# Optimization experiments

Measured on AMD Instinct MI355X. Metric: run time of the kernel, lower is better.

The kernel has to match this reference:

```python
import jax, jax.numpy as jnp
import numpy as np

B, N = 4096, 2048


def setup_inputs() -> dict:
    key = jax.random.key(0)
    k1, k2, k3, k4 = jax.random.split(key, 4)
    return {
        "src_pts3d": jax.random.normal(k1, (B, N, 3), dtype=jnp.float32),
        "tgt_pts3d": jax.random.normal(k2, (B, N, 3), dtype=jnp.float32),
        "kpt_src_mask": jax.random.uniform(k3, (B, N), dtype=jnp.float32),
        "kpt_tgt_mask": jax.random.uniform(k4, (B, N), dtype=jnp.float32),
    }


def reference(src_pts3d, tgt_pts3d, kpt_src_mask, kpt_tgt_mask):
    # H = src^T @ diag(mask_tgt) @ tgt, fused as a masked row-scale contraction: [B,3,3]
    H = jnp.einsum('bnc,bn,bnd->bcd', src_pts3d, kpt_tgt_mask, tgt_pts3d)
    # torch.svd returns V (H = U S V^T); jnp returns Vh, so V = Vh^T
    u, s, vh = jnp.linalg.svd(H)
    v = jnp.swapaxes(vh, -1, -2)              # [B,3,3]
    ut = jnp.swapaxes(u, -1, -2)              # [B,3,3]
    r = v @ ut
    det = jnp.linalg.det(r)                   # [B]
    # branch-free reflection fix: negate 3rd column of V when det(r) < 0
    sign = jnp.where(det < 0, -1.0, 1.0)
    col_scale = jnp.stack([jnp.ones_like(sign), jnp.ones_like(sign), sign], axis=-1)  # [B,3]
    R = (v * col_scale[:, None, :]) @ ut
    return R
```

## Files before the change

### kernel.cpp

```cpp
#include <hip/hip_runtime.h>
#include <math.h>

#define BATCH 4096
#define NPTS  2048
#define THREADS 256
#define BPB 4
#define GRID (BATCH / BPB)

typedef float f32x4 __attribute__((ext_vector_type(4)));

__device__ __forceinline__ f32x4 ntload(const f32x4* p) {
    return __builtin_nontemporal_load(p);
}

#define ACC(sx, sy, sz, tx, ty, tz, mm) do {                                   \
    float d0 = (mm) * (tx), d1 = (mm) * (ty), d2 = (mm) * (tz);                \
    h[0] = fmaf((sx), d0, h[0]); h[1] = fmaf((sx), d1, h[1]); h[2] = fmaf((sx), d2, h[2]); \
    h[3] = fmaf((sy), d0, h[3]); h[4] = fmaf((sy), d1, h[4]); h[5] = fmaf((sy), d2, h[5]); \
    h[6] = fmaf((sz), d0, h[6]); h[7] = fmaf((sz), d1, h[7]); h[8] = fmaf((sz), d2, h[8]); \
} while (0)

#define DECL_HALF(P) f32x4 P##m, P##sa, P##sb, P##sc, P##ta, P##tb, P##tc;

#define LOAD_HALF(P, bb, g) do {                                               \
    const f32x4* s4_ = (const f32x4*)(src  + (size_t)(bb) * (NPTS * 3));       \
    const f32x4* t4_ = (const f32x4*)(tgt  + (size_t)(bb) * (NPTS * 3));       \
    const f32x4* m4_ = (const f32x4*)(mask + (size_t)(bb) * NPTS);             \
    const int g_ = (g);                                                        \
    P##m  = ntload(&m4_[g_]);                                                  \
    P##sa = ntload(&s4_[3 * g_ + 0]);                                          \
    P##sb = ntload(&s4_[3 * g_ + 1]);                                          \
    P##sc = ntload(&s4_[3 * g_ + 2]);                                          \
    P##ta = ntload(&t4_[3 * g_ + 0]);                                          \
    P##tb = ntload(&t4_[3 * g_ + 1]);                                          \
    P##tc = ntload(&t4_[3 * g_ + 2]);                                          \
} while (0)

#define FMA_HALF(P) do {                                                       \
    ACC(P##sa.x, P##sa.y, P##sa.z, P##ta.x, P##ta.y, P##ta.z, P##m.x);         \
    ACC(P##sa.w, P##sb.x, P##sb.y, P##ta.w, P##tb.x, P##tb.y, P##m.y);         \
    ACC(P##sb.z, P##sb.w, P##sc.x, P##tb.z, P##tb.w, P##tc.x, P##m.z);         \
    ACC(P##sc.y, P##sc.z, P##sc.w, P##tc.y, P##tc.z, P##tc.w, P##m.w);         \
} while (0)

__global__ __launch_bounds__(THREADS, 4)
void fused_kernel(const float* __restrict__ src, const float* __restrict__ tgt,
                  const float* __restrict__ mask, float* __restrict__ out)
{
    const int t    = threadIdx.x;
    const int b0   = blockIdx.x * BPB;
    const int wid  = t >> 6;
    const int lane = t & 63;

    __shared__ float shred[BPB][THREADS / 64][9];

    DECL_HALF(A0) DECL_HALF(A1) DECL_HALF(B_)

#define ITER(CUR, NXT, jj, DO_PREF) do {                                       \
    LOAD_HALF(B_, b0 + (jj), t + 256);                                         \
    float h[9] = {0.f, 0.f, 0.f, 0.f, 0.f, 0.f, 0.f, 0.f, 0.f};               \
    FMA_HALF(CUR);                                                             \
    if (DO_PREF) { LOAD_HALF(NXT, b0 + (jj) + 1, t); }                         \
    FMA_HALF(B_);                                                              \
    _Pragma("unroll")                                                          \
    for (int off = 32; off > 0; off >>= 1) {                                   \
        _Pragma("unroll")                                                      \
        for (int i = 0; i < 9; ++i) h[i] += __shfl_down(h[i], off);            \
    }                                                                          \
    if (lane == 0) {                                                           \
        _Pragma("unroll")                                                      \
        for (int i = 0; i < 9; ++i) shred[jj][wid][i] = h[i];                  \
    }                                                                          \
} while (0)

    LOAD_HALF(A0, b0, t);
    ITER(A0, A1, 0, 1);
    ITER(A1, A0, 1, 1);
    ITER(A0, A1, 2, 1);
    ITER(A1, A0, 3, 0);
#undef ITER

    __syncthreads();

    if (t >= BPB) return;

    double H[3][3];
#pragma unroll
    for (int i = 0; i < 9; ++i)
        H[i / 3][i % 3] = (double)(shred[t][0][i] + shred[t][1][i] +
                                   shred[t][2][i] + shred[t][3][i]);

    double A[3][3];
#pragma unroll
    for (int i = 0; i < 3; ++i)
#pragma unroll
        for (int j = 0; j < 3; ++j)
            A[i][j] = H[0][i] * H[0][j] + H[1][i] * H[1][j] + H[2][i] * H[2][j];

    double V[3][3] = {{1, 0, 0}, {0, 1, 0}, {0, 0, 1}};

    for (int sweep = 0; sweep < 6; ++sweep) {
#pragma unroll
        for (int r = 0; r < 3; ++r) {
            const int p = (r == 2) ? 1 : 0;
            const int q = (r == 0) ? 1 : 2;
            const int k = (r == 0) ? 2 : ((r == 1) ? 1 : 0);
            double apq = A[p][q];
            const bool nz = fabs(apq) > 1e-300;
            double theta = (A[q][q] - A[p][p]) / (nz ? 2.0 * apq : 1.0);
            double tt = 1.0 / (fabs(theta) + sqrt(theta * theta + 1.0));
            tt = (theta < 0.0) ? -tt : tt;
            tt = nz ? tt : 0.0;
            double c = 1.0 / sqrt(tt * tt + 1.0);
            double s = tt * c;
            double app = A[p][p], aqq = A[q][q];
            A[p][p] = app - tt * apq;
            A[q][q] = aqq + tt * apq;
            A[p][q] = A[q][p] = 0.0;
            double akp = A[k][p], akq = A[k][q];
            A[k][p] = A[p][k] = c * akp - s * akq;
            A[k][q] = A[q][k] = s * akp + c * akq;
#pragma unroll
            for (int i = 0; i < 3; ++i) {
                double vip = V[i][p], viq = V[i][q];
                V[i][p] = c * vip - s * viq;
                V[i][q] = s * vip + c * viq;
            }
        }
    }

    const double d0 = A[0][0], d1 = A[1][1], d2 = A[2][2];
    const bool g01 = (d0 >= d1);
    const bool g02 = (d0 >= d2);
    const bool g12 = (d1 >= d2);
    const bool l0 = g01 && g02;
    const bool l1 = (!g01) && g12;

    double v0[3], v1[3];
#pragma unroll
    for (int i = 0; i < 3; ++i) {
        const double c0 = V[i][0], c1 = V[i][1], c2 = V[i][2];
        v0[i] = l0 ? c0 : (l1 ? c1 : c2);
        const double s_l0 = g12 ? c1 : c2;
        const double s_l1 = g02 ? c0 : c2;
        const double s_l2 = g01 ? c0 : c1;
        v1[i] = l0 ? s_l0 : (l1 ? s_l1 : s_l2);
    }

    double b0v[3], b1v[3];
#pragma unroll
    for (int r = 0; r < 3; ++r) {
        b0v[r] = H[r][0] * v0[0] + H[r][1] * v0[1] + H[r][2] * v0[2];
        b1v[r] = H[r][0] * v1[0] + H[r][1] * v1[1] + H[r][2] * v1[2];
    }
    double n0 = b0v[0] * b0v[0] + b0v[1] * b0v[1] + b0v[2] * b0v[2];
    double inv0 = 1.0 / sqrt(fmax(n0, 1e-300));
    double u0[3] = {b0v[0] * inv0, b0v[1] * inv0, b0v[2] * inv0};
    double d01 = u0[0] * b1v[0] + u0[1] * b1v[1] + u0[2] * b1v[2];
    double w[3] = {b1v[0] - d01 * u0[0], b1v[1] - d01 * u0[1], b1v[2] - d01 * u0[2]};
    double nw = w[0] * w[0] + w[1] * w[1] + w[2] * w[2];
    double inv1 = 1.0 / sqrt(fmax(nw, 1e-300));
    double u1[3] = {w[0] * inv1, w[1] * inv1, w[2] * inv1};
    double u2[3] = {u0[1] * u1[2] - u0[2] * u1[1],
                    u0[2] * u1[0] - u0[0] * u1[2],
                    u0[0] * u1[1] - u0[1] * u1[0]};
    double vc2[3] = {v0[1] * v1[2] - v0[2] * v1[1],
                     v0[2] * v1[0] - v0[0] * v1[2],
                     v0[0] * v1[1] - v0[1] * v1[0]};

    float* o = out + (size_t)(b0 + t) * 9;
#pragma unroll
    for (int r = 0; r < 3; ++r)
#pragma unroll
        for (int c = 0; c < 3; ++c)
            o[r * 3 + c] = (float)(v0[r] * u0[c] + v1[r] * u1[c] + vc2[r] * u2[c]);
}

extern "C" void kernel_launch(void* const* d_in, const int* in_sizes, int n_in,
                              void* d_out, int out_size, void* d_ws, size_t ws_size,
                              hipStream_t stream) {
    const float* src  = (const float*)d_in[0];
    const float* tgt  = (const float*)d_in[1];
    const float* mask = (const float*)d_in[3];
    float* out = (float*)d_out;

    fused_kernel<<<GRID, THREADS, 0, stream>>>(src, tgt, mask, out);
}
```

Before: 246.1 us.

## Stage coalesced point loads through LDS transpose with double-buffered register prefetch

Replaces strided per-thread loads of 3 float4s at stride 3 with fully contiguous, coalesced float4 loads. The data is written into shared memory with a transposed index so each thread can then read its point triplet back. Work is split into eight half-batch stages, and register-held prefetch of the next stage overlaps the current compute. The intent is better DRAM coalescing, paid for with two barriers per stage and extra LDS traffic.

```diff
diff --git a/kernel.cpp b/kernel.cpp
--- a/kernel.cpp
+++ b/kernel.cpp
@@ -18,29 +18,6 @@
     h[0] = fmaf((sx), d0, h[0]); h[1] = fmaf((sx), d1, h[1]); h[2] = fmaf((sx), d2, h[2]); \
     h[3] = fmaf((sy), d0, h[3]); h[4] = fmaf((sy), d1, h[4]); h[5] = fmaf((sy), d2, h[5]); \
     h[6] = fmaf((sz), d0, h[6]); h[7] = fmaf((sz), d1, h[7]); h[8] = fmaf((sz), d2, h[8]); \
-} while (0)
-
-#define DECL_HALF(P) f32x4 P##m, P##sa, P##sb, P##sc, P##ta, P##tb, P##tc;
-
-#define LOAD_HALF(P, bb, g) do {                                               \
-    const f32x4* s4_ = (const f32x4*)(src  + (size_t)(bb) * (NPTS * 3));       \
-    const f32x4* t4_ = (const f32x4*)(tgt  + (size_t)(bb) * (NPTS * 3));       \
-    const f32x4* m4_ = (const f32x4*)(mask + (size_t)(bb) * NPTS);             \
-    const int g_ = (g);                                                        \
-    P##m  = ntload(&m4_[g_]);                                                  \
-    P##sa = ntload(&s4_[3 * g_ + 0]);                                          \
-    P##sb = ntload(&s4_[3 * g_ + 1]);                                          \
-    P##sc = ntload(&s4_[3 * g_ + 2]);                                          \
-    P##ta = ntload(&t4_[3 * g_ + 0]);                                          \
-    P##tb = ntload(&t4_[3 * g_ + 1]);                                          \
-    P##tc = ntload(&t4_[3 * g_ + 2]);                                          \
-} while (0)
-
-#define FMA_HALF(P) do {                                                       \
-    ACC(P##sa.x, P##sa.y, P##sa.z, P##ta.x, P##ta.y, P##ta.z, P##m.x);         \
-    ACC(P##sa.w, P##sb.x, P##sb.y, P##ta.w, P##tb.x, P##tb.y, P##m.y);         \
-    ACC(P##sb.z, P##sb.w, P##sc.x, P##tb.z, P##tb.w, P##tc.x, P##m.z);         \
-    ACC(P##sc.y, P##sc.z, P##sc.w, P##tc.y, P##tc.z, P##tc.w, P##m.w);         \
 } while (0)
 
 __global__ __launch_bounds__(THREADS, 4)
@@ -52,33 +29,88 @@
     const int wid  = t >> 6;
     const int lane = t & 63;
 
+    __shared__ f32x4 sT[768];
+    __shared__ f32x4 tT[768];
+    __shared__ f32x4 mL[256];
     __shared__ float shred[BPB][THREADS / 64][9];
 
-    DECL_HALF(A0) DECL_HALF(A1) DECL_HALF(B_)
-
-#define ITER(CUR, NXT, jj, DO_PREF) do {                                       \
-    LOAD_HALF(B_, b0 + (jj), t + 256);                                         \
-    float h[9] = {0.f, 0.f, 0.f, 0.f, 0.f, 0.f, 0.f, 0.f, 0.f};               \
-    FMA_HALF(CUR);                                                             \
-    if (DO_PREF) { LOAD_HALF(NXT, b0 + (jj) + 1, t); }                         \
-    FMA_HALF(B_);                                                              \
-    _Pragma("unroll")                                                          \
-    for (int off = 32; off > 0; off >>= 1) {                                   \
+    const f32x4* s4 = (const f32x4*)src;
+    const f32x4* t4 = (const f32x4*)tgt;
+    const f32x4* m4 = (const f32x4*)mask;
+
+    const int w0 = ((t      ) % 3) * 256 + (t      ) / 3;
+    const int w1 = ((t + 256) % 3) * 256 + (t + 256) / 3;
+    const int w2 = ((t + 512) % 3) * 256 + (t + 512) / 3;
+
+    f32x4 As0, As1, As2, At0, At1, At2, Am;
+    f32x4 Bs0, Bs1, Bs2, Bt0, Bt1, Bt2, Bm;
+
+#define GLOAD(P, jj, hh) do {                                                  \
+    const size_t sb_ = (size_t)(b0 + (jj)) * 1536 + (size_t)(hh) * 768;        \
+    const size_t mb_ = (size_t)(b0 + (jj)) * 512  + (size_t)(hh) * 256;        \
+    P##s0 = ntload(&s4[sb_ + t]);                                              \
+    P##s1 = ntload(&s4[sb_ + t + 256]);                                        \
+    P##s2 = ntload(&s4[sb_ + t + 512]);                                        \
+    P##t0 = ntload(&t4[sb_ + t]);                                              \
+    P##t1 = ntload(&t4[sb_ + t + 256]);                                        \
+    P##t2 = ntload(&t4[sb_ + t + 512]);                                        \
+    P##m  = ntload(&m4[mb_ + t]);                                              \
+} while (0)
+
+#define LWRITE(P) do {                                                         \
+    sT[w0] = P##s0; sT[w1] = P##s1; sT[w2] = P##s2;                            \
+    tT[w0] = P##t0; tT[w1] = P##t1; tT[w2] = P##t2;                            \
+    mL[t]  = P##m;                                                             \
+} while (0)
+
+#define CONSUME() do {                                                         \
+    f32x4 sa = sT[t], sbv = sT[256 + t], sc = sT[512 + t];                     \
+    f32x4 ta = tT[t], tbv = tT[256 + t], tc = tT[512 + t];                     \
+    f32x4 mv = mL[t];                                                          \
+    ACC(sa.x,  sa.y,  sa.z,  ta.x,  ta.y,  ta.z,  mv.x);                       \
+    ACC(sa.w,  sbv.x, sbv.y, ta.w,  tbv.x, tbv.y, mv.y);                       \
+    ACC(sbv.z, sbv.w, sc.x,  tbv.z, tbv.w, tc.x,  mv.z);                       \
+    ACC(sc.y,  sc.z,  sc.w,  tc.y,  tc.z,  tc.w,  mv.w);                       \
+} while (0)
+
+    float h[9];
+
+#define ITER(CUR, NXT, jj, hh, PJ, PH, DO_PREF) do {                           \
+    __syncthreads();                      \
+    LWRITE(CUR);                                                               \
+    if (DO_PREF) { GLOAD(NXT, PJ, PH); }        \
+    __syncthreads();                                  \
+    if ((hh) == 0) {                                                           \
         _Pragma("unroll")                                                      \
-        for (int i = 0; i < 9; ++i) h[i] += __shfl_down(h[i], off);            \
+        for (int i = 0; i < 9; ++i) h[i] = 0.f;                                \
     }                                                                          \
-    if (lane == 0) {                                                           \
+    CONSUME();                                                                 \
+    if ((hh) == 1) {                                                           \
         _Pragma("unroll")                                                      \
-        for (int i = 0; i < 9; ++i) shred[jj][wid][i] = h[i];                  \
+        for (int off = 32; off > 0; off >>= 1) {                               \
+            _Pragma("unroll")                                                  \
+            for (int i = 0; i < 9; ++i) h[i] += __shfl_down(h[i], off);        \
+        }                                                                      \
+        if (lane == 0) {                                                       \
+            _Pragma("unroll")                                                  \
+            for (int i = 0; i < 9; ++i) shred[jj][wid][i] = h[i];              \
+        }                                                                      \
     }                                                                          \
 } while (0)
 
-    LOAD_HALF(A0, b0, t);
-    ITER(A0, A1, 0, 1);
-    ITER(A1, A0, 1, 1);
-    ITER(A0, A1, 2, 1);
-    ITER(A1, A0, 3, 0);
+    GLOAD(A, 0, 0);
+    ITER(A, B, 0, 0, 0, 1, 1);
+    ITER(B, A, 0, 1, 1, 0, 1);
+    ITER(A, B, 1, 0, 1, 1, 1);
+    ITER(B, A, 1, 1, 2, 0, 1);
+    ITER(A, B, 2, 0, 2, 1, 1);
+    ITER(B, A, 2, 1, 3, 0, 1);
+    ITER(A, B, 3, 0, 3, 1, 1);
+    ITER(B, A, 3, 1, 0, 0, 0);
 #undef ITER
+#undef CONSUME
+#undef LWRITE
+#undef GLOAD
 
     __syncthreads();
 
```

After: 235.6 us. 1.04x faster.
